# Performance work log

Measured on AMD Instinct MI355X. Metric: run time of the kernel, lower is better.

The kernel has to match this reference:

```python
import jax, jax.numpy as jnp
import numpy as np

C, D, K, N, R = 96, 192, 4, 16, 6  # d_model, d_inner, directions, d_state, dt_rank
B, H, W = 8, 64, 64


def _ln(x, w, b):
    mu = x.mean(-1, keepdims=True)
    var = ((x - mu) ** 2).mean(-1, keepdims=True)
    return (x - mu) * jax.lax.rsqrt(var + 1e-5) * w + b


def setup_inputs() -> dict:
    key = jax.random.key(0)
    ks = jax.random.split(key, 16)
    s = 0.02
    A = jnp.tile(jnp.arange(1, N + 1, dtype=jnp.float32)[None, None, :], (K, D, 1))
    return {
        "x": jax.random.normal(ks[0], (B, C, H, W), jnp.float32),
        "ln1_w": jnp.ones((C,), jnp.float32),
        "ln1_b": jnp.zeros((C,), jnp.float32),
        "in_proj_w": jax.random.normal(ks[1], (2 * D, C), jnp.float32) * s,
        "conv_w": jax.random.normal(ks[2], (D, 1, 3, 3), jnp.float32) * s,
        "conv_b": jnp.zeros((D,), jnp.float32),
        "x_proj_w": jax.random.normal(ks[3], (K, R + 2 * N, D), jnp.float32) * s,
        "dt_projs_w": jax.random.normal(ks[4], (K, D, R), jnp.float32) * s,
        "dt_projs_b": jax.random.normal(ks[5], (K, D), jnp.float32) * 0.1,
        "A_logs": jnp.log(A),
        "Ds": jnp.ones((K, D), jnp.float32),
        "out_norm_w": jnp.ones((D,), jnp.float32),
        "out_norm_b": jnp.zeros((D,), jnp.float32),
        "out_proj_w": jax.random.normal(ks[6], (C, D), jnp.float32) * s,
        "pm_norm_w": jnp.ones((4 * C,), jnp.float32),
        "pm_norm_b": jnp.zeros((4 * C,), jnp.float32),
        "pm_red_w": jax.random.normal(ks[7], (2 * C, 4 * C), jnp.float32) * s,
    }


def reference(x, ln1_w, ln1_b, in_proj_w, conv_w, conv_b, x_proj_w, dt_projs_w,
              dt_projs_b, A_logs, Ds, out_norm_w, out_norm_b, out_proj_w,
              pm_norm_w, pm_norm_b, pm_red_w):
    b, c, h, w = x.shape
    L = h * w
    xh = jnp.transpose(x, (0, 2, 3, 1))  # [B,H,W,C]
    resid = xh
    xn = _ln(xh, ln1_w, ln1_b)
    xz = xn @ in_proj_w.T  # [B,H,W,2D]
    xp, z = xz[..., :D], xz[..., D:]
    xc = jnp.transpose(xp, (0, 3, 1, 2))  # [B,D,H,W]
    xc = jax.lax.conv_general_dilated(
        xc, conv_w, (1, 1), ((1, 1), (1, 1)),
        dimension_numbers=("NCHW", "OIHW", "NCHW"), feature_group_count=D)
    xc = jax.nn.silu(xc + conv_b[None, :, None, None])
    # cross-scan: row-major, col-major, and their reverses -> [B,K,D,L]
    xf = xc.reshape(b, D, L)
    xt = jnp.transpose(xc, (0, 1, 3, 2)).reshape(b, D, L)
    xs = jnp.stack([xf, xt, xf[..., ::-1], xt[..., ::-1]], axis=1)
    x_dbl = jnp.einsum("bkdl,kcd->bkcl", xs, x_proj_w)
    dts = jnp.einsum("bkrl,kdr->bkdl", x_dbl[:, :, :R], dt_projs_w)
    Bs = x_dbl[:, :, R:R + N]  # [B,K,N,L]
    Cs = x_dbl[:, :, R + N:R + 2 * N]
    delta = jax.nn.softplus(dts + dt_projs_b[None, :, :, None])  # [B,K,D,L]
    A = -jnp.exp(A_logs)  # [K,D,N]
    dT = jnp.transpose(delta, (3, 0, 1, 2))  # [L,B,K,D]
    uT = jnp.transpose(xs, (3, 0, 1, 2))
    BT = jnp.transpose(Bs, (3, 0, 1, 2))  # [L,B,K,N]
    CT = jnp.transpose(Cs, (3, 0, 1, 2))
    h0 = jnp.zeros((b, K, D, N), x.dtype)

    def step(hst, inp):
        dt, ut, bt, ct = inp
        hst = hst * jnp.exp(dt[..., None] * A) + (dt * ut)[..., None] * bt[:, :, None, :]
        return hst, jnp.einsum("bkdn,bkn->bkd", hst, ct)

    _, yT = jax.lax.scan(step, h0, (dT, uT, BT, CT))  # yT: [L,B,K,D]
    y = jnp.transpose(yT, (1, 2, 3, 0)) + Ds[None, :, :, None] * xs  # [B,K,D,L]

    def unT(v):  # undo col-major traversal
        return jnp.transpose(v.reshape(b, D, w, h), (0, 1, 3, 2)).reshape(b, D, L)

    yc = y[:, 0] + y[:, 2, :, ::-1] + unT(y[:, 1]) + unT(y[:, 3, :, ::-1])
    yo = jnp.transpose(yc.reshape(b, D, h, w), (0, 2, 3, 1))  # [B,H,W,D]
    yo = _ln(yo, out_norm_w, out_norm_b) * jax.nn.silu(z)
    out = resid + yo @ out_proj_w.T  # [B,H,W,C]
    # PatchMerging2D
    x0 = out[:, 0::2, 0::2]
    x1 = out[:, 1::2, 0::2]
    x2 = out[:, 0::2, 1::2]
    x3 = out[:, 1::2, 1::2]
    xm = jnp.concatenate([x0, x1, x2, x3], -1)  # [B,H/2,W/2,4C]
    xm = _ln(xm, pm_norm_w, pm_norm_b) @ pm_red_w.T  # [B,H/2,W/2,2C]
    return jnp.transpose(xm, (0, 3, 1, 2))
```

## Files before the change

kernel.cpp:

```cpp
#include <hip/hip_runtime.h>
#include <hip/hip_bf16.h>


#define NCH 64
#define CLEN 64

typedef float v2f __attribute__((ext_vector_type(2)));
__device__ __forceinline__ v2f pkfma(v2f a, v2f b, v2f c){ return __builtin_elementwise_fma(a,b,c); }

__device__ __forceinline__ float sigm(float x){ return 1.f/(1.f+__expf(-x)); }
__device__ __forceinline__ float softplus_(float x){ return (x>20.f)? x : __logf(1.f+__expf(x)); }

__device__ __forceinline__ void scan_p0dp2(int k, int v0, int& p0, int& dp){
  if(k==0){ p0 = v0; dp = 1; }
  else if(k==1){ p0 = ((v0&63)<<6)|(v0>>6); dp = 64; }
  else if(k==2){ p0 = 4095 - v0; dp = -1; }
  else { int m0 = 4095 - v0; p0 = ((m0&63)<<6)|(m0>>6); dp = -64; }
}

__global__ __launch_bounds__(256) void k0_prep(
    const float* __restrict__ ipw, const float* __restrict__ xpw,
    const float* __restrict__ dtw, const float* __restrict__ opw,
    const float* __restrict__ pmw,
    float* __restrict__ ipwT, float* __restrict__ xpwTp,
    float* __restrict__ dtwT, float* __restrict__ opwT,
    float* __restrict__ pmwT)
{
  int g = blockIdx.x*256 + threadIdx.x;
  if(g < 36864){
    int c = g/384, n = g%384;
    ipwT[g] = ipw[n*96 + c];
  } else if(g < 67584){
    int t = g - 36864; int dd = t/160, n = t - dd*160; int k = n/40, c = n - k*40;
    float v;
    if(c < 6)       v = xpw[(k*38 + c)*192 + dd];
    else if(c < 8)  v = 0.f;
    else            v = xpw[(k*38 + (c-2))*192 + dd];
    xpwTp[t] = v;
  } else if(g < 72192){
    int t = g - 67584; int kr = t/192, d = t - kr*192; int k = kr/6, r = kr - k*6;
    dtwT[t] = dtw[(k*192 + d)*6 + r];
  } else if(g < 90624){
    int t = g - 72192; int d = t/96, c = t - d*96;
    opwT[t] = opw[c*192 + d];
  } else if(g < 164352){
    int t = g - 90624; int n = t/192, c2 = t - n*192;
    pmwT[t] = pmw[c2*384 + n];
  }
}

#define XT_PAD 68
__global__ __launch_bounds__(256) void k1_ln_inproj(
    const float* __restrict__ x, const float* __restrict__ lnw, const float* __restrict__ lnb,
    const float* __restrict__ ipwT, float* __restrict__ xT,
    float* __restrict__ xp, float* __restrict__ z)
{
  __shared__ float xt[96*XT_PAD];
  __shared__ float lnw_s[96], lnb_s[96], mu_s[64], rs_s[64];
  int tid = threadIdx.x;
  int mt = blockIdx.x, nt = blockIdx.y, b = blockIdx.z;
  int g0 = mt*64;
  const float* xb = x + (size_t)b*96*4096 + g0;
  for(int idx=tid; idx<6144; idx+=256){
    int c = idx>>6, p = idx&63;
    xt[c*XT_PAD+p] = xb[c*4096 + p];
  }
  if(tid<96){ lnw_s[tid]=lnw[tid]; lnb_s[tid]=lnb[tid]; }
  __syncthreads();
  if(nt==0){
    float* xTb = xT + ((size_t)(b*4096 + g0))*96;
    for(int idx=tid; idx<6144; idx+=256){
      int p = idx/96, c = idx - p*96;
      xTb[idx] = xt[c*XT_PAD+p];
    }
  }
  if(tid<64){
    float s=0.f,q=0.f;
    for(int c=0;c<96;c++){ float v=xt[c*XT_PAD+tid]; s+=v; q+=v*v; }
    float mu = s*(1.f/96.f);
    mu_s[tid]=mu; rs_s[tid]=rsqrtf(q*(1.f/96.f)-mu*mu+1e-5f);
  }
  __syncthreads();
  for(int idx=tid; idx<6144; idx+=256){
    int c = idx>>6, p = idx&63;
    int a = c*XT_PAD+p;
    xt[a] = (xt[a]-mu_s[p])*rs_s[p]*lnw_s[c]+lnb_s[c];
  }
  __syncthreads();
  int tm = tid>>5, tn = tid&31;
  float acc[8][4];
  #pragma unroll
  for(int i=0;i<8;i++){acc[i][0]=0.f;acc[i][1]=0.f;acc[i][2]=0.f;acc[i][3]=0.f;}
  const float* wbase = ipwT + nt*128 + tn*4;
  for(int kk=0;kk<96;kk++){
    float4 w4 = *(const float4*)(wbase + kk*384);
    float4 a0 = *(const float4*)&xt[kk*XT_PAD + tm*8];
    float4 a1 = *(const float4*)&xt[kk*XT_PAD + tm*8 + 4];
    float av[8]={a0.x,a0.y,a0.z,a0.w,a1.x,a1.y,a1.z,a1.w};
    #pragma unroll
    for(int i=0;i<8;i++){
      acc[i][0]=fmaf(av[i],w4.x,acc[i][0]);
      acc[i][1]=fmaf(av[i],w4.y,acc[i][1]);
      acc[i][2]=fmaf(av[i],w4.z,acc[i][2]);
      acc[i][3]=fmaf(av[i],w4.w,acc[i][3]);
    }
  }
  int n = nt*128 + tn*4;
  #pragma unroll
  for(int i=0;i<8;i++){
    size_t row = (size_t)(b*4096 + g0 + tm*8 + i);
    float4 v = make_float4(acc[i][0],acc[i][1],acc[i][2],acc[i][3]);
    if(n < 192) *(float4*)(xp + row*192 + n) = v;
    else        *(float4*)(z  + row*192 + (n-192)) = v;
  }
}

__global__ __launch_bounds__(192) void k2_conv(
    const float* __restrict__ xp, const float* __restrict__ cw, const float* __restrict__ cb,
    float* __restrict__ xc)
{
  __shared__ float cw_s[1728];
  int tid = threadIdx.x;
  int pq = blockIdx.x, b = blockIdx.y;
  for(int i=tid;i<1728;i+=192) cw_s[i]=cw[i];
  __syncthreads();
  int th = (pq>>3)<<1;
  int tw = (pq&7)<<3;
  const float* base = xp + (size_t)b*4096*192 + tid;
  const float* wp = &cw_s[tid*9];
  float bias = cb[tid];
  float acc[2][8];
  #pragma unroll
  for(int r=0;r<2;r++)
    #pragma unroll
    for(int j=0;j<8;j++) acc[r][j]=bias;
  #pragma unroll
  for(int iy=0; iy<4; iy++){
    int hh = th-1+iy;
    if(hh<0||hh>63) continue;
    float v[10];
    #pragma unroll
    for(int xx=0;xx<10;xx++){
      int ww = tw-1+xx;
      v[xx] = (ww>=0 && ww<64) ? base[((size_t)(hh*64+ww))*192] : 0.f;
    }
    #pragma unroll
    for(int r=0;r<2;r++){
      int ky = iy - r;
      if(ky<0||ky>2) continue;
      float wk0=wp[ky*3], wk1=wp[ky*3+1], wk2=wp[ky*3+2];
      #pragma unroll
      for(int j=0;j<8;j++)
        acc[r][j] = fmaf(v[j],wk0, fmaf(v[j+1],wk1, fmaf(v[j+2],wk2, acc[r][j])));
    }
  }
  #pragma unroll
  for(int r=0;r<2;r++)
    #pragma unroll
    for(int j=0;j<8;j++){
      float a = acc[r][j];
      a = a * sigm(a);
      xc[((size_t)(b*4096) + (th+r)*64 + tw+j)*192 + tid] = a;
    }
}

__global__ __launch_bounds__(320) void k3_proj(
    const float* __restrict__ xc, const float* __restrict__ xpwTp,
    float* __restrict__ xdbl)
{
  __shared__ float sm[32*192];
  int tid = threadIdx.x;
  int mt = blockIdx.x, b = blockIdx.y;
  int g0 = mt*32;
  const float* xcb = xc + ((size_t)(b*4096 + g0))*192;
  for(int idx=tid; idx<6144; idx+=320) sm[idx] = xcb[idx];
  __syncthreads();
  int tn = tid%40, tm = tid/40;
  float acc[4][4];
  #pragma unroll
  for(int i=0;i<4;i++){acc[i][0]=0.f;acc[i][1]=0.f;acc[i][2]=0.f;acc[i][3]=0.f;}
  const float* wb = xpwTp + tn*4;
  for(int kk=0;kk<192;kk+=2){
    float4 w0 = *(const float4*)(wb + kk*160);
    float4 w1 = *(const float4*)(wb + (kk+1)*160);
    #pragma unroll
    for(int i=0;i<4;i++){
      float2 a = *(const float2*)&sm[(tm*4+i)*192 + kk];
      acc[i][0] = fmaf(a.x,w0.x, fmaf(a.y,w1.x, acc[i][0]));
      acc[i][1] = fmaf(a.x,w0.y, fmaf(a.y,w1.y, acc[i][1]));
      acc[i][2] = fmaf(a.x,w0.z, fmaf(a.y,w1.z, acc[i][2]));
      acc[i][3] = fmaf(a.x,w0.w, fmaf(a.y,w1.w, acc[i][3]));
    }
  }
  #pragma unroll
  for(int i=0;i<4;i++){
    *(float4*)(xdbl + ((size_t)(b*4096 + g0 + tm*4 + i))*160 + tn*4)
      = make_float4(acc[i][0],acc[i][1],acc[i][2],acc[i][3]);
  }
}

__global__ __launch_bounds__(192) void k4a_scanlocal(
    const float* __restrict__ xdbl, const float* __restrict__ xc,
    const float* __restrict__ alog, const float* __restrict__ dtwT,
    const float* __restrict__ dtb,
    float* __restrict__ localH, float* __restrict__ Ssum)
{
  int d = threadIdx.x;
  int ch = blockIdx.x, k = blockIdx.y, b = blockIdx.z;
  size_t prow = (size_t)b*4096;
  int p0, dp;
  scan_p0dp2(k, ch*CLEN, p0, dp);
  const float* rowp = xdbl + (prow + (size_t)p0)*160 + k*40;
  ptrdiff_t rstride = (ptrdiff_t)dp*160;
  float w0=dtwT[(k*6+0)*192+d], w1=dtwT[(k*6+1)*192+d], w2=dtwT[(k*6+2)*192+d],
        w3=dtwT[(k*6+3)*192+d], w4=dtwT[(k*6+4)*192+d], w5=dtwT[(k*6+5)*192+d];
  float dtbv = dtb[k*192+d];
  float A0; bool fast1;
  {
    const float4* ap = (const float4*)(alog + (size_t)(k*192+d)*16);
    float4 a0=ap[0],a1=ap[1],a2=ap[2],a3=ap[3];
    float t[16]={a0.x,a0.y,a0.z,a0.w,a1.x,a1.y,a1.z,a1.w,a2.x,a2.y,a2.z,a2.w,a3.x,a3.y,a3.z,a3.w};
    A0 = -__expf(t[0]);
    bool fast = true;
    #pragma unroll
    for(int n=1;n<16;n++)
      fast = fast && (fabsf(-__expf(t[n]) - (float)(n+1)*A0) <= 1e-4f*(float)(n+1)*fabsf(A0));
    fast1 = fast && (A0 == -1.0f);
  }
  float S=0.f;
  const float* xu = xc + (prow + (size_t)p0)*192 + d;
  ptrdiff_t ustride = (ptrdiff_t)dp*192;
  if(fast1){
    v2f h01={0.f,0.f},h23={0.f,0.f},h45={0.f,0.f},h67={0.f,0.f},
        h89={0.f,0.f},hAB={0.f,0.f},hCD={0.f,0.f},hEF={0.f,0.f};
    for(int i=0;i<CLEN;i++){
      const float* row = rowp; rowp += rstride;
      float u = *xu; xu += ustride;
      float4 r03 = *(const float4*)row;
      float2 r45 = *(const float2*)(row+4);
      float p01 = fmaf(r03.y,w1, r03.x*w0);
      float p23 = fmaf(r03.w,w3, r03.z*w2);
      float p45 = fmaf(r45.y,w5, r45.x*w4);
      float raw = (dtbv + p01) + (p23 + p45);
      float ex = __expf(raw);
      float tt = 1.f + ex;
      float delta = (raw>20.f)? raw : __logf(tt);
      float e1 = __builtin_amdgcn_rcpf(tt);
      float du = delta*u;
      S += delta;
      float4 B0=*(const float4*)(row+8),  B1=*(const float4*)(row+12),
             B2=*(const float4*)(row+16), B3=*(const float4*)(row+20);
      float e2s = e1*e1;
      v2f e2v = {e2s,e2s};
      v2f e4v = e2v*e2v;
      v2f e8v = e4v*e4v;
      v2f c01 = {e1,e2s};
      v2f c23 = c01*e2v;
      v2f c45 = c01*e4v;
      v2f c67 = c23*e4v;
      v2f c89 = c01*e8v;
      v2f cAB = c23*e8v;
      v2f cCD = c45*e8v;
      v2f cEF = c67*e8v;
      v2f du2 = {du,du};
      h01 = pkfma(h01,c01, du2*(v2f){B0.x,B0.y});
      h23 = pkfma(h23,c23, du2*(v2f){B0.z,B0.w});
      h45 = pkfma(h45,c45, du2*(v2f){B1.x,B1.y});
      h67 = pkfma(h67,c67, du2*(v2f){B1.z,B1.w});
      h89 = pkfma(h89,c89, du2*(v2f){B2.x,B2.y});
      hAB = pkfma(hAB,cAB, du2*(v2f){B2.z,B2.w});
      hCD = pkfma(hCD,cCD, du2*(v2f){B3.x,B3.y});
      hEF = pkfma(hEF,cEF, du2*(v2f){B3.z,B3.w});
    }
    float* lh = localH + ((((size_t)(b*4+k))*NCH + ch)*192 + d)*16;
    *(float4*)(lh+0)  = make_float4(h01.x,h01.y,h23.x,h23.y);
    *(float4*)(lh+4)  = make_float4(h45.x,h45.y,h67.x,h67.y);
    *(float4*)(lh+8)  = make_float4(h89.x,h89.y,hAB.x,hAB.y);
    *(float4*)(lh+12) = make_float4(hCD.x,hCD.y,hEF.x,hEF.y);
  } else {
    float A[16], h[16];
    {
      const float4* ap = (const float4*)(alog + (size_t)(k*192+d)*16);
      float4 a0=ap[0],a1=ap[1],a2=ap[2],a3=ap[3];
      float t[16]={a0.x,a0.y,a0.z,a0.w,a1.x,a1.y,a1.z,a1.w,a2.x,a2.y,a2.z,a2.w,a3.x,a3.y,a3.z,a3.w};
      #pragma unroll
      for(int n=0;n<16;n++){ A[n] = -__expf(t[n]); h[n]=0.f; }
    }
    for(int i=0;i<CLEN;i++){
      const float* row = rowp; rowp += rstride;
      float u = *xu; xu += ustride;
      float p01 = fmaf(row[1],w1, row[0]*w0);
      float p23 = fmaf(row[3],w3, row[2]*w2);
      float p45 = fmaf(row[5],w5, row[4]*w4);
      float delta = softplus_((dtbv + p01) + (p23 + p45));
      float du = delta*u;
      S += delta;
      float4 B0=*(const float4*)(row+8),  B1=*(const float4*)(row+12),
             B2=*(const float4*)(row+16), B3=*(const float4*)(row+20);
      float Bn[16]={B0.x,B0.y,B0.z,B0.w,B1.x,B1.y,B1.z,B1.w,
                    B2.x,B2.y,B2.z,B2.w,B3.x,B3.y,B3.z,B3.w};
      #pragma unroll
      for(int n=0;n<16;n++) h[n] = fmaf(h[n], __expf(delta*A[n]), du*Bn[n]);
    }
    float* lh = localH + ((((size_t)(b*4+k))*NCH + ch)*192 + d)*16;
    #pragma unroll
    for(int n4=0;n4<4;n4++)
      *(float4*)(lh + n4*4) = make_float4(h[n4*4],h[n4*4+1],h[n4*4+2],h[n4*4+3]);
  }
  Ssum[(((size_t)(b*4+k))*NCH + ch)*192 + d] = S;
}

__global__ __launch_bounds__(256) void k4b_chain(
    float* __restrict__ localH, const float* __restrict__ Ssum,
    const float* __restrict__ alog)
{
  int g = blockIdx.x*256 + threadIdx.x;
  int bk = g/3072, dn = g - bk*3072;
  int k = bk & 3;
  int d = dn>>4, n = dn&15;
  float A = -__expf(alog[((size_t)(k*192+d))*16 + n]);
  size_t hbase = (size_t)bk*NCH*3072 + dn;
  size_t sbase = (size_t)bk*NCH*192 + d;
  float hv = 0.f;
  float loc = localH[hbase];
  float S   = Ssum[sbase];
  for(int ch=0; ch<NCH; ch++){
    float nloc = 0.f, nS = 0.f;
    if(ch < NCH-1){
      nloc = localH[hbase + (size_t)(ch+1)*3072];
      nS   = Ssum[sbase + (size_t)(ch+1)*192];
    }
    float dec = __expf(A*S);
    localH[hbase + (size_t)ch*3072] = hv;
    hv = fmaf(hv, dec, loc);
    loc = nloc; S = nS;
  }
}

__global__ __launch_bounds__(192) void k4c_scanfull(
    const float* __restrict__ xdbl, const float* __restrict__ xc,
    const float* __restrict__ alog, const float* __restrict__ dtwT,
    const float* __restrict__ dtb, const float* __restrict__ hin,
    const float* __restrict__ Dsv, __hip_bfloat16* __restrict__ yB)
{
  int d = threadIdx.x;
  int ch = blockIdx.x, k = blockIdx.y, b = blockIdx.z;
  size_t prow = (size_t)b*4096;
  int p0, dp;
  scan_p0dp2(k, ch*CLEN, p0, dp);
  const float* rowp = xdbl + (prow + (size_t)p0)*160 + k*40;
  ptrdiff_t rstride = (ptrdiff_t)dp*160;
  float w0=dtwT[(k*6+0)*192+d], w1=dtwT[(k*6+1)*192+d], w2=dtwT[(k*6+2)*192+d],
        w3=dtwT[(k*6+3)*192+d], w4=dtwT[(k*6+4)*192+d], w5=dtwT[(k*6+5)*192+d];
  float dtbv = dtb[k*192+d];
  float A0; bool fast1;
  {
    const float4* ap = (const float4*)(alog + (size_t)(k*192+d)*16);
    float4 a0=ap[0],a1=ap[1],a2=ap[2],a3=ap[3];
    float t[16]={a0.x,a0.y,a0.z,a0.w,a1.x,a1.y,a1.z,a1.w,a2.x,a2.y,a2.z,a2.w,a3.x,a3.y,a3.z,a3.w};
    A0 = -__expf(t[0]);
    bool fast = true;
    #pragma unroll
    for(int n=1;n<16;n++)
      fast = fast && (fabsf(-__expf(t[n]) - (float)(n+1)*A0) <= 1e-4f*(float)(n+1)*fabsf(A0));
    fast1 = fast && (A0 == -1.0f);
  }
  float dsv = Dsv[k*192+d];
  const float* xu = xc + (prow + (size_t)p0)*192 + d;
  ptrdiff_t ustride = (ptrdiff_t)dp*192;
  __hip_bfloat16* yP = yB + (((size_t)(b*4+k))*4096 + ch*CLEN)*192 + d;
  const float* hp = hin + ((((size_t)(b*4+k))*NCH + ch)*192 + d)*16;
  if(fast1){
    float4 h0=((const float4*)hp)[0], h1=((const float4*)hp)[1],
           h2=((const float4*)hp)[2], h3=((const float4*)hp)[3];
    v2f h01={h0.x,h0.y}, h23={h0.z,h0.w}, h45={h1.x,h1.y}, h67={h1.z,h1.w},
        h89={h2.x,h2.y}, hAB={h2.z,h2.w}, hCD={h3.x,h3.y}, hEF={h3.z,h3.w};
    for(int i=0;i<CLEN;i++){
      const float* row = rowp; rowp += rstride;
      float u = *xu; xu += ustride;
      float4 r03 = *(const float4*)row;
      float2 r45 = *(const float2*)(row+4);
      float p01 = fmaf(r03.y,w1, r03.x*w0);
      float p23 = fmaf(r03.w,w3, r03.z*w2);
      float p45 = fmaf(r45.y,w5, r45.x*w4);
      float raw = (dtbv + p01) + (p23 + p45);
      float ex = __expf(raw);
      float tt = 1.f + ex;
      float delta = (raw>20.f)? raw : __logf(tt);
      float e1 = __builtin_amdgcn_rcpf(tt);
      float du = delta*u;
      float4 B0=*(const float4*)(row+8),  B1=*(const float4*)(row+12),
             B2=*(const float4*)(row+16), B3=*(const float4*)(row+20);
      float4 C0=*(const float4*)(row+24), C1=*(const float4*)(row+28),
             C2=*(const float4*)(row+32), C3=*(const float4*)(row+36);
      float e2s = e1*e1;
      v2f e2v = {e2s,e2s};
      v2f e4v = e2v*e2v;
      v2f e8v = e4v*e4v;
      v2f c01 = {e1,e2s};
      v2f c23 = c01*e2v;
      v2f c45 = c01*e4v;
      v2f c67 = c23*e4v;
      v2f c89 = c01*e8v;
      v2f cAB = c23*e8v;
      v2f cCD = c45*e8v;
      v2f cEF = c67*e8v;
      v2f du2 = {du,du};
      h01 = pkfma(h01,c01, du2*(v2f){B0.x,B0.y});
      h23 = pkfma(h23,c23, du2*(v2f){B0.z,B0.w});
      h45 = pkfma(h45,c45, du2*(v2f){B1.x,B1.y});
      h67 = pkfma(h67,c67, du2*(v2f){B1.z,B1.w});
      h89 = pkfma(h89,c89, du2*(v2f){B2.x,B2.y});
      hAB = pkfma(hAB,cAB, du2*(v2f){B2.z,B2.w});
      hCD = pkfma(hCD,cCD, du2*(v2f){B3.x,B3.y});
      hEF = pkfma(hEF,cEF, du2*(v2f){B3.z,B3.w});
      v2f yv = h01*(v2f){C0.x,C0.y};
      yv = pkfma(h23,(v2f){C0.z,C0.w}, yv);
      yv = pkfma(h45,(v2f){C1.x,C1.y}, yv);
      yv = pkfma(h67,(v2f){C1.z,C1.w}, yv);
      yv = pkfma(h89,(v2f){C2.x,C2.y}, yv);
      yv = pkfma(hAB,(v2f){C2.z,C2.w}, yv);
      yv = pkfma(hCD,(v2f){C3.x,C3.y}, yv);
      yv = pkfma(hEF,(v2f){C3.z,C3.w}, yv);
      yP[(size_t)i*192] = __float2bfloat16(fmaf(dsv, u, yv.x + yv.y));
    }
  } else {
    float A[16], h[16];
    {
      const float4* ap = (const float4*)(alog + (size_t)(k*192+d)*16);
      float4 a0=ap[0],a1=ap[1],a2=ap[2],a3=ap[3];
      float t[16]={a0.x,a0.y,a0.z,a0.w,a1.x,a1.y,a1.z,a1.w,a2.x,a2.y,a2.z,a2.w,a3.x,a3.y,a3.z,a3.w};
      #pragma unroll
      for(int n=0;n<16;n++) A[n] = -__expf(t[n]);
    }
    {
      float4 h0=((const float4*)hp)[0], h1=((const float4*)hp)[1],
             h2=((const float4*)hp)[2], h3=((const float4*)hp)[3];
      h[0]=h0.x;h[1]=h0.y;h[2]=h0.z;h[3]=h0.w;h[4]=h1.x;h[5]=h1.y;h[6]=h1.z;h[7]=h1.w;
      h[8]=h2.x;h[9]=h2.y;h[10]=h2.z;h[11]=h2.w;h[12]=h3.x;h[13]=h3.y;h[14]=h3.z;h[15]=h3.w;
    }
    for(int i=0;i<CLEN;i++){
      const float* row = rowp; rowp += rstride;
      float u = *xu; xu += ustride;
      float p01 = fmaf(row[1],w1, row[0]*w0);
      float p23 = fmaf(row[3],w3, row[2]*w2);
      float p45 = fmaf(row[5],w5, row[4]*w4);
      float delta = softplus_((dtbv + p01) + (p23 + p45));
      float du = delta*u;
      float4 B0=*(const float4*)(row+8),  B1=*(const float4*)(row+12),
             B2=*(const float4*)(row+16), B3=*(const float4*)(row+20);
      float Bn[16]={B0.x,B0.y,B0.z,B0.w,B1.x,B1.y,B1.z,B1.w,
                    B2.x,B2.y,B2.z,B2.w,B3.x,B3.y,B3.z,B3.w};
      float4 C0=*(const float4*)(row+24), C1=*(const float4*)(row+28),
             C2=*(const float4*)(row+32), C3=*(const float4*)(row+36);
      float Cn[16]={C0.x,C0.y,C0.z,C0.w,C1.x,C1.y,C1.z,C1.w,
                    C2.x,C2.y,C2.z,C2.w,C3.x,C3.y,C3.z,C3.w};
      float y = 0.f;
      #pragma unroll
      for(int n=0;n<16;n++){
        h[n] = fmaf(h[n], __expf(delta*A[n]), du*Bn[n]);
        y = fmaf(h[n], Cn[n], y);
      }
      yP[(size_t)i*192] = __float2bfloat16(fmaf(dsv, u, y));
    }
  }
}

#define YPAD 193
__global__ __launch_bounds__(256) void k5_combine(
    const __hip_bfloat16* __restrict__ yS, const float* __restrict__ z, const float* __restrict__ xT,
    const float* __restrict__ onw, const float* __restrict__ onb,
    const float* __restrict__ opwT, float* __restrict__ out_pre)
{
  __shared__ float yn[64*YPAD];
  __shared__ float wsm[48*96];
  __shared__ float mu_s[64], rs_s[64];
  int tid = threadIdx.x;
  int mt = blockIdx.x, b = blockIdx.y;
  int g0 = mt*64;
  size_t base = (size_t)b*4*4096;
  for(int idx=tid; idx<12288; idx+=256){
    int p = idx/192, d = idx - p*192;
    int gp = g0 + p;
    int l1 = ((gp&63)<<6)|(gp>>6);
    float v = __bfloat162float(yS[(base + gp)*192 + d])
            + __bfloat162float(yS[(base + 4096 + l1)*192 + d])
            + __bfloat162float(yS[(base + 2*4096 + (4095-gp))*192 + d])
            + __bfloat162float(yS[(base + 3*4096 + (4095-l1))*192 + d]);
    yn[p*YPAD+d] = v;
  }
  __syncthreads();
  {
    int p = tid>>2, q = tid&3;
    float s=0.f, sq=0.f;
    for(int c=q;c<192;c+=4){ float v=yn[p*YPAD+c]; s+=v; sq=fmaf(v,v,sq); }
    s  += __shfl_xor(s,1);  sq += __shfl_xor(sq,1);
    s  += __shfl_xor(s,2);  sq += __shfl_xor(sq,2);
    if(q==0){
      float mu = s*(1.f/192.f);
      mu_s[p]=mu; rs_s[p]=rsqrtf(sq*(1.f/192.f)-mu*mu+1e-5f);
    }
  }
  __syncthreads();
  for(int idx=tid; idx<12288; idx+=256){
    int p = idx/192, d = idx - p*192;
    float zz = z[((size_t)(b*4096+g0+p))*192 + d];
    float v = (yn[p*YPAD+d]-mu_s[p])*rs_s[p]*onw[d]+onb[d];
    yn[p*YPAD+d] = v * zz * sigm(zz);
  }
  __syncthreads();
  int tn = tid&15, tm = tid>>4;
  float acc[4][6];
  #pragma unroll
  for(int i=0;i<4;i++)
    #pragma unroll
    for(int j=0;j<6;j++) acc[i][j]=0.f;
  for(int kc=0; kc<4; kc++){
    for(int idx=tid; idx<4608; idx+=256) wsm[idx] = opwT[kc*4608 + idx];
    __syncthreads();
    for(int kk=0;kk<48;kk++){
      float a0 = yn[(tm*4+0)*YPAD + kc*48+kk];
      float a1 = yn[(tm*4+1)*YPAD + kc*48+kk];
      float a2 = yn[(tm*4+2)*YPAD + kc*48+kk];
      float a3 = yn[(tm*4+3)*YPAD + kc*48+kk];
      const float* wr = &wsm[kk*96 + tn*6];
      #pragma unroll
      for(int j=0;j<6;j++){
        float w = wr[j];
        acc[0][j]=fmaf(a0,w,acc[0][j]);
        acc[1][j]=fmaf(a1,w,acc[1][j]);
        acc[2][j]=fmaf(a2,w,acc[2][j]);
        acc[3][j]=fmaf(a3,w,acc[3][j]);
      }
    }
    __syncthreads();
  }
  #pragma unroll
  for(int i=0;i<4;i++){
    size_t row = (size_t)(b*4096 + g0 + tm*4 + i);
    const float* xr = xT + row*96 + tn*6;
    float* orr = out_pre + row*96 + tn*6;
    #pragma unroll
    for(int j=0;j<6;j++) orr[j] = acc[i][j] + xr[j];
  }
}

__global__ __launch_bounds__(192) void k6_pm(
    const float* __restrict__ out_pre, const float* __restrict__ pmw, const float* __restrict__ pmb,
    const float* __restrict__ pmwT, float* __restrict__ outp)
{
  __shared__ float xm[8*388];
  __shared__ float xo[8*193];
  __shared__ float mus[8], rss[8];
  int tid = threadIdx.x;
  int jt = blockIdx.x, i = blockIdx.y, b = blockIdx.z;
  for(int idx=tid; idx<3072; idx+=192){
    int pj = idx/384, n = idx - pj*384;
    int q = n/96, c = n - q*96;
    int j = jt*8 + pj;
    int h2 = 2*i + (q&1), w2 = 2*j + (q>>1);
    xm[pj*388+n] = out_pre[((size_t)b*4096 + h2*64 + w2)*96 + c];
  }
  __syncthreads();
  if(tid<8){
    float s=0.f,q=0.f;
    for(int n=0;n<384;n++){ float v=xm[tid*388+n]; s+=v; q+=v*v; }
    float mu=s*(1.f/384.f);
    mus[tid]=mu; rss[tid]=rsqrtf(q*(1.f/384.f)-mu*mu+1e-5f);
  }
  __syncthreads();
  for(int idx=tid; idx<3072; idx+=192){
    int pj = idx/384, n = idx - pj*384;
    xm[pj*388+n] = (xm[pj*388+n]-mus[pj])*rss[pj]*pmw[n]+pmb[n];
  }
  __syncthreads();
  float acc[8];
  #pragma unroll
  for(int pj=0;pj<8;pj++) acc[pj]=0.f;
  const float* wb = pmwT + tid;
  for(int n4=0;n4<96;n4++){
    float w0=wb[(n4*4+0)*192], w1=wb[(n4*4+1)*192], w2=wb[(n4*4+2)*192], w3=wb[(n4*4+3)*192];
    #pragma unroll
    for(int pj=0;pj<8;pj++){
      float4 v = *(const float4*)&xm[pj*388 + n4*4];
      acc[pj] = fmaf(v.x,w0,fmaf(v.y,w1,fmaf(v.z,w2,fmaf(v.w,w3,acc[pj]))));
    }
  }
  #pragma unroll
  for(int pj=0;pj<8;pj++) xo[pj*193+tid]=acc[pj];
  __syncthreads();
  for(int idx=tid; idx<1536; idx+=192){
    int c2 = idx>>3, pj = idx&7;
    outp[(((size_t)b*192 + c2)*32 + i)*32 + jt*8 + pj] = xo[pj*193+c2];
  }
}

extern "C" void kernel_launch(void* const* d_in, const int* in_sizes, int n_in,
                              void* d_out, int out_size, void* d_ws, size_t ws_size,
                              hipStream_t stream)
{
  const float* x    = (const float*)d_in[0];
  const float* lnw  = (const float*)d_in[1];
  const float* lnb  = (const float*)d_in[2];
  const float* ipw  = (const float*)d_in[3];
  const float* cw   = (const float*)d_in[4];
  const float* cb   = (const float*)d_in[5];
  const float* xpw  = (const float*)d_in[6];
  const float* dtw  = (const float*)d_in[7];
  const float* dtb  = (const float*)d_in[8];
  const float* alog = (const float*)d_in[9];
  const float* Dsv  = (const float*)d_in[10];
  const float* onw  = (const float*)d_in[11];
  const float* onb  = (const float*)d_in[12];
  const float* opw  = (const float*)d_in[13];
  const float* pmnw = (const float*)d_in[14];
  const float* pmnb = (const float*)d_in[15];
  const float* pmrw = (const float*)d_in[16];
  float* out = (float*)d_out;

  float* ws    = (float*)d_ws;
  float* xT    = ws;
  float* xpb   = xT + 3145728;
  float* zb    = xpb + 6291456;
  float* xcb   = zb + 6291456;
  float* yBf   = xcb + 6291456;
  float* lH    = yBf + 12582912;
  float* Ss    = lH + 6291456;
  float* ipwT  = Ss + 393216;
  float* xpwTp = ipwT + 36864;
  float* dtwT  = xpwTp + 30720;
  float* opwT  = dtwT + 4608;
  float* pmwT  = opwT + 18432;
  float* xdbl  = xpb;
  float* outp  = xpb;
  __hip_bfloat16* yB = (__hip_bfloat16*)yBf;

  k0_prep      <<<dim3(642),      dim3(256), 0, stream>>>(ipw,xpw,dtw,opw,pmrw, ipwT,xpwTp,dtwT,opwT,pmwT);
  k1_ln_inproj <<<dim3(64,3,8),   dim3(256), 0, stream>>>(x,lnw,lnb,ipwT, xT,xpb,zb);
  k2_conv      <<<dim3(256,8),    dim3(192), 0, stream>>>(xpb,cw,cb, xcb);
  k3_proj      <<<dim3(128,8),    dim3(320), 0, stream>>>(xcb,xpwTp, xdbl);
  k4a_scanlocal<<<dim3(NCH,4,8),  dim3(192), 0, stream>>>(xdbl,xcb,alog,dtwT,dtb, lH,Ss);
  k4b_chain    <<<dim3(384),      dim3(256), 0, stream>>>(lH,Ss,alog);
  k4c_scanfull <<<dim3(NCH,4,8),  dim3(192), 0, stream>>>(xdbl,xcb,alog,dtwT,dtb,lH,Dsv, yB);
  k5_combine   <<<dim3(64,8),     dim3(256), 0, stream>>>(yB,zb,xT,onw,onb,opwT, outp);
  k6_pm        <<<dim3(4,32,8),   dim3(192), 0, stream>>>(outp,pmnw,pmnb,pmwT, out);
}
```

Baseline: 318.6 us.

## Store conv output and chunk-local scan states in bf16

The conv activation buffer xc and the per-chunk local scan states localH are now stored as bf16 rather than fp32, and every reader converts back to float. This halves the memory traffic for these intermediates across the conv, x_proj, both scan passes and the chain kernel. In exchange it adds conversion work and reduces the precision of the scan input and of the carried hidden states, which could push the output error up.

```diff
diff --git a/kernel.cpp b/kernel.cpp
--- a/kernel.cpp
+++ b/kernel.cpp
@@ -10,6 +10,14 @@
 
 __device__ __forceinline__ float sigm(float x){ return 1.f/(1.f+__expf(-x)); }
 __device__ __forceinline__ float softplus_(float x){ return (x>20.f)? x : __logf(1.f+__expf(x)); }
+
+__device__ __forceinline__ unsigned packbf2(float a, float b){
+  __hip_bfloat16 ba = __float2bfloat16(a), bb = __float2bfloat16(b);
+  unsigned short ua = *(unsigned short*)&ba, ub = *(unsigned short*)&bb;
+  return (unsigned)ua | ((unsigned)ub<<16);
+}
+__device__ __forceinline__ float unpk_lo(unsigned u){ return __uint_as_float((u&0xffffu)<<16); }
+__device__ __forceinline__ float unpk_hi(unsigned u){ return __uint_as_float(u&0xffff0000u); }
 
 __device__ __forceinline__ void scan_p0dp2(int k, int v0, int& p0, int& dp){
   if(k==0){ p0 = v0; dp = 1; }
@@ -117,7 +125,7 @@
 
 __global__ __launch_bounds__(192) void k2_conv(
     const float* __restrict__ xp, const float* __restrict__ cw, const float* __restrict__ cb,
-    float* __restrict__ xc)
+    __hip_bfloat16* __restrict__ xc)
 {
   __shared__ float cw_s[1728];
   int tid = threadIdx.x;
@@ -160,20 +168,24 @@
     for(int j=0;j<8;j++){
       float a = acc[r][j];
       a = a * sigm(a);
-      xc[((size_t)(b*4096) + (th+r)*64 + tw+j)*192 + tid] = a;
+      xc[((size_t)(b*4096) + (th+r)*64 + tw+j)*192 + tid] = __float2bfloat16(a);
     }
 }
 
 __global__ __launch_bounds__(320) void k3_proj(
-    const float* __restrict__ xc, const float* __restrict__ xpwTp,
+    const __hip_bfloat16* __restrict__ xc, const float* __restrict__ xpwTp,
     float* __restrict__ xdbl)
 {
   __shared__ float sm[32*192];
   int tid = threadIdx.x;
   int mt = blockIdx.x, b = blockIdx.y;
   int g0 = mt*32;
-  const float* xcb = xc + ((size_t)(b*4096 + g0))*192;
-  for(int idx=tid; idx<6144; idx+=320) sm[idx] = xcb[idx];
+  const unsigned* xcb = (const unsigned*)(xc + ((size_t)(b*4096 + g0))*192);
+  for(int idx=tid; idx<3072; idx+=320){
+    unsigned u = xcb[idx];
+    sm[idx*2]   = unpk_lo(u);
+    sm[idx*2+1] = unpk_hi(u);
+  }
   __syncthreads();
   int tn = tid%40, tm = tid/40;
   float acc[4][4];
@@ -200,10 +212,10 @@
 }
 
 __global__ __launch_bounds__(192) void k4a_scanlocal(
-    const float* __restrict__ xdbl, const float* __restrict__ xc,
+    const float* __restrict__ xdbl, const __hip_bfloat16* __restrict__ xc,
     const float* __restrict__ alog, const float* __restrict__ dtwT,
     const float* __restrict__ dtb,
-    float* __restrict__ localH, float* __restrict__ Ssum)
+    __hip_bfloat16* __restrict__ localH, float* __restrict__ Ssum)
 {
   int d = threadIdx.x;
   int ch = blockIdx.x, k = blockIdx.y, b = blockIdx.z;
@@ -228,14 +240,15 @@
     fast1 = fast && (A0 == -1.0f);
   }
   float S=0.f;
-  const float* xu = xc + (prow + (size_t)p0)*192 + d;
+  const __hip_bfloat16* xu = xc + (prow + (size_t)p0)*192 + d;
   ptrdiff_t ustride = (ptrdiff_t)dp*192;
+  unsigned* lh = (unsigned*)(localH + ((((size_t)(b*4+k))*NCH + ch)*192 + d)*16);
   if(fast1){
     v2f h01={0.f,0.f},h23={0.f,0.f},h45={0.f,0.f},h67={0.f,0.f},
         h89={0.f,0.f},hAB={0.f,0.f},hCD={0.f,0.f},hEF={0.f,0.f};
     for(int i=0;i<CLEN;i++){
       const float* row = rowp; rowp += rstride;
-      float u = *xu; xu += ustride;
+      float u = __bfloat162float(*xu); xu += ustride;
       float4 r03 = *(const float4*)row;
       float2 r45 = *(const float2*)(row+4);
       float p01 = fmaf(r03.y,w1, r03.x*w0);
@@ -272,11 +285,13 @@
       hCD = pkfma(hCD,cCD, du2*(v2f){B3.x,B3.y});
       hEF = pkfma(hEF,cEF, du2*(v2f){B3.z,B3.w});
     }
-    float* lh = localH + ((((size_t)(b*4+k))*NCH + ch)*192 + d)*16;
-    *(float4*)(lh+0)  = make_float4(h01.x,h01.y,h23.x,h23.y);
-    *(float4*)(lh+4)  = make_float4(h45.x,h45.y,h67.x,h67.y);
-    *(float4*)(lh+8)  = make_float4(h89.x,h89.y,hAB.x,hAB.y);
-    *(float4*)(lh+12) = make_float4(hCD.x,hCD.y,hEF.x,hEF.y);
+    uint4 q0, q1;
+    q0.x = packbf2(h01.x,h01.y); q0.y = packbf2(h23.x,h23.y);
+    q0.z = packbf2(h45.x,h45.y); q0.w = packbf2(h67.x,h67.y);
+    q1.x = packbf2(h89.x,h89.y); q1.y = packbf2(hAB.x,hAB.y);
+    q1.z = packbf2(hCD.x,hCD.y); q1.w = packbf2(hEF.x,hEF.y);
+    *(uint4*)lh = q0;
+    *(uint4*)(lh+4) = q1;
   } else {
     float A[16], h[16];
     {
@@ -288,7 +303,7 @@
     }
     for(int i=0;i<CLEN;i++){
       const float* row = rowp; rowp += rstride;
-      float u = *xu; xu += ustride;
+      float u = __bfloat162float(*xu); xu += ustride;
       float p01 = fmaf(row[1],w1, row[0]*w0);
       float p23 = fmaf(row[3],w3, row[2]*w2);
       float p45 = fmaf(row[5],w5, row[4]*w4);
@@ -302,16 +317,19 @@
       #pragma unroll
       for(int n=0;n<16;n++) h[n] = fmaf(h[n], __expf(delta*A[n]), du*Bn[n]);
     }
-    float* lh = localH + ((((size_t)(b*4+k))*NCH + ch)*192 + d)*16;
-    #pragma unroll
-    for(int n4=0;n4<4;n4++)
-      *(float4*)(lh + n4*4) = make_float4(h[n4*4],h[n4*4+1],h[n4*4+2],h[n4*4+3]);
+    uint4 q0, q1;
+    q0.x = packbf2(h[0],h[1]);   q0.y = packbf2(h[2],h[3]);
+    q0.z = packbf2(h[4],h[5]);   q0.w = packbf2(h[6],h[7]);
+    q1.x = packbf2(h[8],h[9]);   q1.y = packbf2(h[10],h[11]);
+    q1.z = packbf2(h[12],h[13]); q1.w = packbf2(h[14],h[15]);
+    *(uint4*)lh = q0;
+    *(uint4*)(lh+4) = q1;
   }
   Ssum[(((size_t)(b*4+k))*NCH + ch)*192 + d] = S;
 }
 
 __global__ __launch_bounds__(256) void k4b_chain(
-    float* __restrict__ localH, const float* __restrict__ Ssum,
+    __hip_bfloat16* __restrict__ localH, const float* __restrict__ Ssum,
     const float* __restrict__ alog)
 {
   int g = blockIdx.x*256 + threadIdx.x;
@@ -322,25 +340,25 @@
   size_t hbase = (size_t)bk*NCH*3072 + dn;
   size_t sbase = (size_t)bk*NCH*192 + d;
   float hv = 0.f;
-  float loc = localH[hbase];
+  float loc = __bfloat162float(localH[hbase]);
   float S   = Ssum[sbase];
   for(int ch=0; ch<NCH; ch++){
     float nloc = 0.f, nS = 0.f;
     if(ch < NCH-1){
-      nloc = localH[hbase + (size_t)(ch+1)*3072];
+      nloc = __bfloat162float(localH[hbase + (size_t)(ch+1)*3072]);
       nS   = Ssum[sbase + (size_t)(ch+1)*192];
     }
     float dec = __expf(A*S);
-    localH[hbase + (size_t)ch*3072] = hv;
+    localH[hbase + (size_t)ch*3072] = __float2bfloat16(hv);
     hv = fmaf(hv, dec, loc);
     loc = nloc; S = nS;
   }
 }
 
 __global__ __launch_bounds__(192) void k4c_scanfull(
-    const float* __restrict__ xdbl, const float* __restrict__ xc,
+    const float* __restrict__ xdbl, const __hip_bfloat16* __restrict__ xc,
     const float* __restrict__ alog, const float* __restrict__ dtwT,
-    const float* __restrict__ dtb, const float* __restrict__ hin,
+    const float* __restrict__ dtb, const __hip_bfloat16* __restrict__ hin,
     const float* __restrict__ Dsv, __hip_bfloat16* __restrict__ yB)
 {
   int d = threadIdx.x;
@@ -366,18 +384,20 @@
     fast1 = fast && (A0 == -1.0f);
   }
   float dsv = Dsv[k*192+d];
-  const float* xu = xc + (prow + (size_t)p0)*192 + d;
+  const __hip_bfloat16* xu = xc + (prow + (size_t)p0)*192 + d;
   ptrdiff_t ustride = (ptrdiff_t)dp*192;
   __hip_bfloat16* yP = yB + (((size_t)(b*4+k))*4096 + ch*CLEN)*192 + d;
-  const float* hp = hin + ((((size_t)(b*4+k))*NCH + ch)*192 + d)*16;
+  const unsigned* hp = (const unsigned*)(hin + ((((size_t)(b*4+k))*NCH + ch)*192 + d)*16);
+  uint4 q0 = *(const uint4*)hp;
+  uint4 q1 = *(const uint4*)(hp+4);
   if(fast1){
-    float4 h0=((const float4*)hp)[0], h1=((const float4*)hp)[1],
-           h2=((const float4*)hp)[2], h3=((const float4*)hp)[3];
-    v2f h01={h0.x,h0.y}, h23={h0.z,h0.w}, h45={h1.x,h1.y}, h67={h1.z,h1.w},
-        h89={h2.x,h2.y}, hAB={h2.z,h2.w}, hCD={h3.x,h3.y}, hEF={h3.z,h3.w};
+    v2f h01={unpk_lo(q0.x),unpk_hi(q0.x)}, h23={unpk_lo(q0.y),unpk_hi(q0.y)},
+        h45={unpk_lo(q0.z),unpk_hi(q0.z)}, h67={unpk_lo(q0.w),unpk_hi(q0.w)},
+        h89={unpk_lo(q1.x),unpk_hi(q1.x)}, hAB={unpk_lo(q1.y),unpk_hi(q1.y)},
+        hCD={unpk_lo(q1.z),unpk_hi(q1.z)}, hEF={unpk_lo(q1.w),unpk_hi(q1.w)};
     for(int i=0;i<CLEN;i++){
       const float* row = rowp; rowp += rstride;
-      float u = *xu; xu += ustride;
+      float u = __bfloat162float(*xu); xu += ustride;
       float4 r03 = *(const float4*)row;
       float2 r45 = *(const float2*)(row+4);
       float p01 = fmaf(r03.y,w1, r03.x*w0);
@@ -433,15 +453,13 @@
       #pragma unroll
       for(int n=0;n<16;n++) A[n] = -__expf(t[n]);
     }
-    {
-      float4 h0=((const float4*)hp)[0], h1=((const float4*)hp)[1],
-             h2=((const float4*)hp)[2], h3=((const float4*)hp)[3];
-      h[0]=h0.x;h[1]=h0.y;h[2]=h0.z;h[3]=h0.w;h[4]=h1.x;h[5]=h1.y;h[6]=h1.z;h[7]=h1.w;
-      h[8]=h2.x;h[9]=h2.y;h[10]=h2.z;h[11]=h2.w;h[12]=h3.x;h[13]=h3.y;h[14]=h3.z;h[15]=h3.w;
-    }
+    h[0]=unpk_lo(q0.x); h[1]=unpk_hi(q0.x); h[2]=unpk_lo(q0.y); h[3]=unpk_hi(q0.y);
+    h[4]=unpk_lo(q0.z); h[5]=unpk_hi(q0.z); h[6]=unpk_lo(q0.w); h[7]=unpk_hi(q0.w);
+    h[8]=unpk_lo(q1.x); h[9]=unpk_hi(q1.x); h[10]=unpk_lo(q1.y); h[11]=unpk_hi(q1.y);
+    h[12]=unpk_lo(q1.z); h[13]=unpk_hi(q1.z); h[14]=unpk_lo(q1.w); h[15]=unpk_hi(q1.w);
     for(int i=0;i<CLEN;i++){
       const float* row = rowp; rowp += rstride;
-      float u = *xu; xu += ustride;
+      float u = __bfloat162float(*xu); xu += ustride;
       float p01 = fmaf(row[1],w1, row[0]*w0);
       float p23 = fmaf(row[3],w3, row[2]*w2);
       float p45 = fmaf(row[5],w5, row[4]*w4);
@@ -622,10 +640,10 @@
   float* xT    = ws;
   float* xpb   = xT + 3145728;
   float* zb    = xpb + 6291456;
-  float* xcb   = zb + 6291456;
-  float* yBf   = xcb + 6291456;
-  float* lH    = yBf + 12582912;
-  float* Ss    = lH + 6291456;
+  float* xcf   = zb + 6291456;
+  float* yBf   = xcf + 3145728;
+  float* lHf   = yBf + 12582912;
+  float* Ss    = lHf + 3145728;
   float* ipwT  = Ss + 393216;
   float* xpwTp = ipwT + 36864;
   float* dtwT  = xpwTp + 30720;
@@ -633,15 +651,17 @@
   float* pmwT  = opwT + 18432;
   float* xdbl  = xpb;
   float* outp  = xpb;
+  __hip_bfloat16* xc = (__hip_bfloat16*)xcf;
   __hip_bfloat16* yB = (__hip_bfloat16*)yBf;
+  __hip_bfloat16* lH = (__hip_bfloat16*)lHf;
 
   k0_prep      <<<dim3(642),      dim3(256), 0, stream>>>(ipw,xpw,dtw,opw,pmrw, ipwT,xpwTp,dtwT,opwT,pmwT);
   k1_ln_inproj <<<dim3(64,3,8),   dim3(256), 0, stream>>>(x,lnw,lnb,ipwT, xT,xpb,zb);
-  k2_conv      <<<dim3(256,8),    dim3(192), 0, stream>>>(xpb,cw,cb, xcb);
-  k3_proj      <<<dim3(128,8),    dim3(320), 0, stream>>>(xcb,xpwTp, xdbl);
-  k4a_scanlocal<<<dim3(NCH,4,8),  dim3(192), 0, stream>>>(xdbl,xcb,alog,dtwT,dtb, lH,Ss);
+  k2_conv      <<<dim3(256,8),    dim3(192), 0, stream>>>(xpb,cw,cb, xc);
+  k3_proj      <<<dim3(128,8),    dim3(320), 0, stream>>>(xc,xpwTp, xdbl);
+  k4a_scanlocal<<<dim3(NCH,4,8),  dim3(192), 0, stream>>>(xdbl,xc,alog,dtwT,dtb, lH,Ss);
   k4b_chain    <<<dim3(384),      dim3(256), 0, stream>>>(lH,Ss,alog);
-  k4c_scanfull <<<dim3(NCH,4,8),  dim3(192), 0, stream>>>(xdbl,xcb,alog,dtwT,dtb,lH,Dsv, yB);
+  k4c_scanfull <<<dim3(NCH,4,8),  dim3(192), 0, stream>>>(xdbl,xc,alog,dtwT,dtb,lH,Dsv, yB);
   k5_combine   <<<dim3(64,8),     dim3(256), 0, stream>>>(yB,zb,xT,onw,onb,opwT, outp);
   k6_pm        <<<dim3(4,32,8),   dim3(192), 0, stream>>>(outp,pmnw,pmnb,pmwT, out);
 }
```

After: 315.5 us. Within noise of the previous version (-0.9%).
